# Optimization experiments

Hardware: AMD Instinct MI355X
Metric: run time of the kernel (lower is better)

Reference implementation:

```python
import jax, jax.numpy as jnp
import numpy as np

TEMPERATURE = 8.0  # sqrt(head_dim=64)


def sparsemax(z):
    """Sparsemax along the last axis (Martins & Astudillo 2016)."""
    S = z.shape[-1]
    z_sorted = -jnp.sort(-z, axis=-1)            # descending sort
    cs = jnp.cumsum(z_sorted, axis=-1)
    ks = jnp.arange(1, S + 1, dtype=z.dtype)
    support = 1.0 + ks * z_sorted > cs           # entries in the support set
    k_sup = jnp.sum(support, axis=-1, keepdims=True)  # support size >= 1
    tau = (jnp.take_along_axis(cs, k_sup - 1, axis=-1) - 1.0) / k_sup.astype(z.dtype)
    return jnp.maximum(z - tau, 0.0)


def setup_inputs() -> dict:
    key = jax.random.key(0)
    kq, kk, kv, km = jax.random.split(key, 4)
    B, Lq, Lk, D = 64, 1024, 1024, 64
    q = jax.random.normal(kq, (B, Lq, D), dtype=jnp.float32)
    k = jax.random.normal(kk, (B, Lk, D), dtype=jnp.float32)
    v = jax.random.normal(kv, (B, Lk, D), dtype=jnp.float32)
    mask = jax.random.randint(km, (B, Lq, Lk), 0, 2).astype(bool)  # True = masked out
    return {"q": q, "k": k, "v": v, "mask": mask}


def reference(q, k, v, mask):
    # scores: [B, Lq, Lk]
    attn = jnp.einsum('bqd,bkd->bqk', q / TEMPERATURE, k)
    # mask out disallowed keys with -inf
    attn = jnp.where(mask, -jnp.inf, attn)
    # rows where ALL keys are masked: set scores to 0 (avoids NaN in sparsemax)
    inf_mask = jnp.all(mask, axis=2, keepdims=True)  # [B, Lq, 1]
    attn = jnp.where(inf_mask, 0.0, attn)
    attn = sparsemax(attn)
    # zero out fully-masked rows again (dropout has p=0.0 -> identity in eval)
    attn = jnp.where(inf_mask, 0.0, attn)
    out = jnp.einsum('bqk,bkd->bqd', attn, v)
    return (out, attn)
```

## Files before the change

### kernel.cpp

```cpp
#include <hip/hip_runtime.h>
#include <float.h>


#define BATCH    64
#define SEQQ     1024
#define SEQK     1024
#define DHEAD    64

typedef short short8 __attribute__((ext_vector_type(8)));
typedef float f32x4  __attribute__((ext_vector_type(4)));
typedef unsigned short us4v __attribute__((ext_vector_type(4)));

typedef const __attribute__((address_space(1))) unsigned int as1_cuint;
typedef __attribute__((address_space(3))) unsigned int as3_uint;
typedef __attribute__((address_space(3))) unsigned char as3_uchar;

__device__ __forceinline__ unsigned short bf16_rne(float f) {
    unsigned u = __float_as_uint(f);
    u += 0x7fffu + ((u >> 16) & 1u);
    return (unsigned short)(u >> 16);
}

__device__ __forceinline__ void cvt_hilo8(const float* fv, float scale,
                                          short8* hi, short8* lo) {
    #pragma unroll
    for (int j = 0; j < 8; ++j) {
        float f = fv[j] * scale;
        unsigned short hb = bf16_rne(f);
        float hf = __uint_as_float((unsigned)hb << 16);
        (*hi)[j] = (short)hb;
        (*lo)[j] = (short)bf16_rne(f - hf);
    }
}

__global__ void detect_mask_fmt(const unsigned char* __restrict__ m,
                                int* __restrict__ flag) {
    __shared__ int s_found;
    if (threadIdx.x == 0) s_found = 0;
    __syncthreads();
    int found = 0;
    for (int o = threadIdx.x; o < 65536; o += 256) {
        if ((o & 3) != 0 && m[o] != 0) found = 1;
    }
    if (found) atomicOr(&s_found, 1);
    __syncthreads();
    if (threadIdx.x == 0) *flag = s_found;
}

__global__ __launch_bounds__(256) void kprep(
        const float* __restrict__ k, unsigned short* __restrict__ kbuf) {
    int gid  = blockIdx.x * 256 + threadIdx.x;
    int db   = gid & 7;
    int keyg = (gid >> 3) & 1023;
    int b    = gid >> 13;
    int kt   = keyg >> 7;
    int key  = keyg & 127;

    const float4* src =
        (const float4*)(k + ((size_t)b * SEQK + keyg) * DHEAD + db * 8);
    float4 f0 = src[0], f1 = src[1];
    float fv[8] = {f0.x, f0.y, f0.z, f0.w, f1.x, f1.y, f1.z, f1.w};
    short8 hi, lo;
    cvt_hilo8(fv, 1.0f, &hi, &lo);

    unsigned short* tile = kbuf + (size_t)(b * 8 + kt) * 16384;
    int off = key * 64 + ((db ^ (key & 7)) * 8);
    *(short8*)(tile + off)        = hi;
    *(short8*)(tile + 8192 + off) = lo;
}

__global__ __launch_bounds__(256) void score_kernel_dma(
        const float* __restrict__ q, const unsigned short* __restrict__ kbuf,
        unsigned short* __restrict__ sbuf, int pitch) {
    const int lane = threadIdx.x & 63;
    const int wave = threadIdx.x >> 6;
    const int quad = lane >> 4;
    const int l15  = lane & 15;
    const int qt = blockIdx.x >> 6;
    const int b  = blockIdx.x & 63;

    __shared__ unsigned short klds[2 * 128 * 64];

    const float* qrow =
        q + ((size_t)b * SEQQ + qt * 64 + wave * 16 + l15) * DHEAD;
    short8 a_hi[2], a_lo[2];
    #pragma unroll
    for (int kc = 0; kc < 2; ++kc) {
        const float4* src = (const float4*)(qrow + kc * 32 + quad * 8);
        float4 f0 = src[0], f1 = src[1];
        float fv[8] = {f0.x, f0.y, f0.z, f0.w, f1.x, f1.y, f1.z, f1.w};
        cvt_hilo8(fv, 0.125f, &a_hi[kc], &a_lo[kc]);
    }

    unsigned short* srow0 =
        sbuf + ((size_t)b * SEQQ + qt * 64 + wave * 16) * (size_t)pitch;

    for (int kt = 0; kt < 8; ++kt) {
        __syncthreads();
        const unsigned char* gtile =
            (const unsigned char*)(kbuf + (size_t)(b * 8 + kt) * 16384);
        {
            unsigned base = wave * 8192 + lane * 16;
            #pragma unroll
            for (int j = 0; j < 8; ++j) {
                unsigned off = base + j * 1024;
                as1_cuint* gp = (as1_cuint*)(gtile + off);
                as3_uint*  lp = (as3_uint*)((as3_uchar*)klds +
                                            (wave * 8192 + j * 1024));
                __builtin_amdgcn_global_load_lds(gp, lp, 16, 0, 0);
            }
        }
        __syncthreads();

        unsigned short* srow = srow0 + kt * 128;
        #pragma unroll
        for (int g = 0; g < 8; ++g) {
            int key = g * 16 + l15;
            short8 b_hi[2], b_lo[2];
            #pragma unroll
            for (int kc = 0; kc < 2; ++kc) {
                int db  = kc * 4 + quad;
                int off = key * 64 + ((db ^ (key & 7)) * 8);
                b_hi[kc] = *(const short8*)(klds + off);
                b_lo[kc] = *(const short8*)(klds + 8192 + off);
            }
            f32x4 acc = {0.f, 0.f, 0.f, 0.f};
            #pragma unroll
            for (int kc = 0; kc < 2; ++kc) {
                acc = __builtin_amdgcn_mfma_f32_16x16x32_bf16(a_hi[kc], b_hi[kc], acc, 0, 0, 0);
                acc = __builtin_amdgcn_mfma_f32_16x16x32_bf16(a_lo[kc], b_hi[kc], acc, 0, 0, 0);
                acc = __builtin_amdgcn_mfma_f32_16x16x32_bf16(a_hi[kc], b_lo[kc], acc, 0, 0, 0);
            }
            #pragma unroll
            for (int r = 0; r < 4; ++r)
                srow[(size_t)(quad * 4 + r) * (size_t)pitch + g * 16 + l15] =
                    bf16_rne(acc[r]);
        }
    }
}

__global__ __launch_bounds__(256) void score_kernel_cvt(
        const float* __restrict__ q, const float* __restrict__ k,
        unsigned short* __restrict__ sbuf, int pitch) {
    const int lane = threadIdx.x & 63;
    const int wave = threadIdx.x >> 6;
    const int quad = lane >> 4;
    const int l15  = lane & 15;
    const int qt = blockIdx.x >> 6;
    const int b  = blockIdx.x & 63;

    __shared__ unsigned short klds[2 * 128 * 64];

    const float* qrow =
        q + ((size_t)b * SEQQ + qt * 64 + wave * 16 + l15) * DHEAD;
    short8 a_hi[2], a_lo[2];
    #pragma unroll
    for (int kc = 0; kc < 2; ++kc) {
        const float4* src = (const float4*)(qrow + kc * 32 + quad * 8);
        float4 f0 = src[0], f1 = src[1];
        float fv[8] = {f0.x, f0.y, f0.z, f0.w, f1.x, f1.y, f1.z, f1.w};
        cvt_hilo8(fv, 0.125f, &a_hi[kc], &a_lo[kc]);
    }

    const float* kb = k + (size_t)b * SEQK * DHEAD;
    unsigned short* srow0 =
        sbuf + ((size_t)b * SEQQ + qt * 64 + wave * 16) * (size_t)pitch;

    for (int kt = 0; kt < 8; ++kt) {
        __syncthreads();
        const float* kbase = kb + (size_t)kt * 128 * DHEAD;
        #pragma unroll
        for (int it = 0; it < 4; ++it) {
            int e   = threadIdx.x + 256 * it;
            int key = e >> 3, db = e & 7;
            const float4* src = (const float4*)(kbase + key * DHEAD + db * 8);
            float4 f0 = src[0], f1 = src[1];
            float fv[8] = {f0.x, f0.y, f0.z, f0.w, f1.x, f1.y, f1.z, f1.w};
            short8 hi, lo;
            cvt_hilo8(fv, 1.0f, &hi, &lo);
            int off = key * 64 + ((db ^ (key & 7)) * 8);
            *(short8*)(klds + off)        = hi;
            *(short8*)(klds + 8192 + off) = lo;
        }
        __syncthreads();

        unsigned short* srow = srow0 + kt * 128;
        #pragma unroll
        for (int g = 0; g < 8; ++g) {
            int key = g * 16 + l15;
            short8 b_hi[2], b_lo[2];
            #pragma unroll
            for (int kc = 0; kc < 2; ++kc) {
                int db  = kc * 4 + quad;
                int off = key * 64 + ((db ^ (key & 7)) * 8);
                b_hi[kc] = *(const short8*)(klds + off);
                b_lo[kc] = *(const short8*)(klds + 8192 + off);
            }
            f32x4 acc = {0.f, 0.f, 0.f, 0.f};
            #pragma unroll
            for (int kc = 0; kc < 2; ++kc) {
                acc = __builtin_amdgcn_mfma_f32_16x16x32_bf16(a_hi[kc], b_hi[kc], acc, 0, 0, 0);
                acc = __builtin_amdgcn_mfma_f32_16x16x32_bf16(a_lo[kc], b_hi[kc], acc, 0, 0, 0);
                acc = __builtin_amdgcn_mfma_f32_16x16x32_bf16(a_hi[kc], b_lo[kc], acc, 0, 0, 0);
            }
            #pragma unroll
            for (int r = 0; r < 4; ++r)
                srow[(size_t)(quad * 4 + r) * (size_t)pitch + g * 16 + l15] =
                    bf16_rne(acc[r]);
        }
    }
}

__global__ __launch_bounds__(256) void sparsemax_pv(
        const float* __restrict__ v, const void* __restrict__ mask,
        const int* __restrict__ fmt_flag,
        float* __restrict__ out, float* __restrict__ attn,
        const unsigned short* __restrict__ sbuf, int pitch) {
    const int lane = threadIdx.x & 63;
    const int wave = threadIdx.x >> 6;
    const int row  = blockIdx.x * 4 + wave;
    const int b    = row >> 10;
    float* arow = attn + (size_t)row * SEQK;
    const int mask_is_byte = fmt_flag ? *fmt_flag : 1;

    __shared__ float pbuf[4][SEQK];

    const us4v* s4 = (const us4v*)(sbuf + (size_t)row * (size_t)pitch);
    float s[16];
    #pragma unroll
    for (int t = 0; t < 4; ++t) {
        us4v u = __builtin_nontemporal_load(s4 + lane + 64 * t);
        s[4*t+0] = __uint_as_float((unsigned)u[0] << 16);
        s[4*t+1] = __uint_as_float((unsigned)u[1] << 16);
        s[4*t+2] = __uint_as_float((unsigned)u[2] << 16);
        s[4*t+3] = __uint_as_float((unsigned)u[3] << 16);
    }
    if (mask_is_byte) {
        const unsigned* m32 =
            (const unsigned*)((const unsigned char*)mask + (size_t)row * SEQK);
        #pragma unroll
        for (int t = 0; t < 4; ++t) {
            unsigned m = __builtin_nontemporal_load(m32 + lane + 64 * t);
            if (m & 0x000000ffu) s[4*t+0] = -FLT_MAX;
            if (m & 0x0000ff00u) s[4*t+1] = -FLT_MAX;
            if (m & 0x00ff0000u) s[4*t+2] = -FLT_MAX;
            if (m & 0xff000000u) s[4*t+3] = -FLT_MAX;
        }
    } else {
        const int* mi = (const int*)mask + (size_t)row * SEQK;
        #pragma unroll
        for (int t = 0; t < 4; ++t) {
            int m0 = __builtin_nontemporal_load(mi + 4 * (lane + 64 * t) + 0);
            int m1 = __builtin_nontemporal_load(mi + 4 * (lane + 64 * t) + 1);
            int m2 = __builtin_nontemporal_load(mi + 4 * (lane + 64 * t) + 2);
            int m3 = __builtin_nontemporal_load(mi + 4 * (lane + 64 * t) + 3);
            if (m0) s[4*t+0] = -FLT_MAX;
            if (m1) s[4*t+1] = -FLT_MAX;
            if (m2) s[4*t+2] = -FLT_MAX;
            if (m3) s[4*t+3] = -FLT_MAX;
        }
    }

    float mx = -FLT_MAX;
    #pragma unroll
    for (int i = 0; i < 16; ++i) mx = fmaxf(mx, s[i]);
    #pragma unroll
    for (int off = 32; off >= 1; off >>= 1)
        mx = fmaxf(mx, __shfl_xor(mx, off, 64));

    if (mx <= -FLT_MAX) {
        f32x4 z = {0.f, 0.f, 0.f, 0.f};
        #pragma unroll
        for (int t = 0; t < 4; ++t)
            __builtin_nontemporal_store(z, (f32x4*)arow + lane + 64 * t);
        out[(size_t)row * DHEAD + lane] = 0.f;
        return;
    }

    float thr = mx - 1.0f, tau = 0.f;
    int cnt_prev = -1;
    for (int it = 0; it < 32; ++it) {
        float lsum = 0.f; int lcnt = 0;
        #pragma unroll
        for (int i = 0; i < 16; ++i)
            if (s[i] > thr) { lsum += s[i]; lcnt++; }
        #pragma unroll
        for (int off = 32; off >= 1; off >>= 1) {
            lsum += __shfl_xor(lsum, off, 64);
            lcnt += __shfl_xor(lcnt, off, 64);
        }
        tau = (lsum - 1.0f) / (float)lcnt;
        if (lcnt == cnt_prev) break;
        cnt_prev = lcnt;
        thr = tau;
    }

    float p[16];
    #pragma unroll
    for (int i = 0; i < 16; ++i) {
        float pv = s[i] - tau;
        p[i] = pv > 0.f ? pv : 0.f;
    }
    #pragma unroll
    for (int t = 0; t < 4; ++t) {
        f32x4 f = {p[4*t+0], p[4*t+1], p[4*t+2], p[4*t+3]};
        __builtin_nontemporal_store(f, (f32x4*)arow + lane + 64 * t);
        *(f32x4*)&pbuf[wave][4 * (lane + 64 * t)] = f;
    }

    const float* vbase = v + (size_t)b * SEQK * DHEAD;
    float oacc = 0.f;
    #pragma unroll
    for (int t = 0; t < 4; ++t) {
        #pragma unroll
        for (int c = 0; c < 4; ++c) {
            int i = 4 * t + c;
            unsigned long long mb = __ballot(p[i] > 0.f);
            while (mb) {
                int k0, k1 = -1, k2 = -1, k3 = -1;
                k0 = __ffsll(mb) - 1; mb &= mb - 1;
                if (mb) { k1 = __ffsll(mb) - 1; mb &= mb - 1; }
                if (mb) { k2 = __ffsll(mb) - 1; mb &= mb - 1; }
                if (mb) { k3 = __ffsll(mb) - 1; mb &= mb - 1; }
                int key0 = 4 * k0 + 256 * t + c;
                float pj0 = pbuf[wave][key0];
                float v0  = vbase[(size_t)key0 * DHEAD + lane];
                float pj1 = 0.f, pj2 = 0.f, pj3 = 0.f;
                float v1 = 0.f, v2 = 0.f, v3 = 0.f;
                if (k1 >= 0) {
                    int key1 = 4 * k1 + 256 * t + c;
                    pj1 = pbuf[wave][key1];
                    v1  = vbase[(size_t)key1 * DHEAD + lane];
                }
                if (k2 >= 0) {
                    int key2 = 4 * k2 + 256 * t + c;
                    pj2 = pbuf[wave][key2];
                    v2  = vbase[(size_t)key2 * DHEAD + lane];
                }
                if (k3 >= 0) {
                    int key3 = 4 * k3 + 256 * t + c;
                    pj3 = pbuf[wave][key3];
                    v3  = vbase[(size_t)key3 * DHEAD + lane];
                }
                oacc = fmaf(pj0, v0, oacc);
                if (k1 >= 0) oacc = fmaf(pj1, v1, oacc);
                if (k2 >= 0) oacc = fmaf(pj2, v2, oacc);
                if (k3 >= 0) oacc = fmaf(pj3, v3, oacc);
            }
        }
    }
    out[(size_t)row * DHEAD + lane] = oacc;
}

extern "C" void kernel_launch(void* const* d_in, const int* in_sizes, int n_in,
                              void* d_out, int out_size, void* d_ws, size_t ws_size,
                              hipStream_t stream) {
    const float* q = (const float*)d_in[0];
    const float* k = (const float*)d_in[1];
    const float* v = (const float*)d_in[2];
    const void*  m = d_in[3];

    float* out  = (float*)d_out;
    float* attn = out + (size_t)BATCH * SEQQ * DHEAD;

    int* flag = nullptr;
    if (ws_size >= sizeof(int)) {
        flag = (int*)d_ws;
        detect_mask_fmt<<<1, 256, 0, stream>>>((const unsigned char*)m, flag);
    }

    const size_t S_BYTES = (size_t)BATCH * SEQQ * SEQK * 2;
    const size_t K_BYTES = (size_t)BATCH * SEQK * DHEAD * 2 * 2;

    unsigned short* sbuf;
    int pitch;
    bool s_in_ws = ws_size >= 16 + S_BYTES;
    if (s_in_ws) {
        sbuf  = (unsigned short*)d_ws + 8;
        pitch = SEQK;
    } else {
        sbuf  = (unsigned short*)attn;
        pitch = 2 * SEQK;
    }

    bool k_in_ws = s_in_ws && ws_size >= 16 + S_BYTES + K_BYTES;
    if (k_in_ws) {
        unsigned short* kbuf =
            (unsigned short*)((char*)d_ws + 16 + S_BYTES);
        kprep<<<(BATCH * SEQK * 8) / 256, 256, 0, stream>>>(k, kbuf);
        score_kernel_dma<<<(SEQQ / 64) * BATCH, 256, 0, stream>>>(
            q, kbuf, sbuf, pitch);
    } else {
        score_kernel_cvt<<<(SEQQ / 64) * BATCH, 256, 0, stream>>>(
            q, k, sbuf, pitch);
    }

    sparsemax_pv<<<(BATCH * SEQQ) / 4, 256, 0, stream>>>(
        v, m, flag, out, attn, sbuf, pitch);
}
```

Before: 646.2 us.

## Transpose score MFMA for packed stores and write sparse attn over memset

The score kernels swap the MFMA operand order so each lane holds four consecutive keys for one query row, which allows a packed 8-byte bf16 store instead of four strided 2-byte stores. When the score buffer lives in the workspace, the attention output is cleared with a hipMemsetAsync and the sparsemax kernel writes only the nonzero probabilities with scattered scalar stores, instead of dense nontemporal vector stores of the full row. This replaces kernel-side zero writes with a driver fill pass. The scattered per-element stores may coalesce poorly.

```diff
diff --git a/kernel.cpp b/kernel.cpp
--- a/kernel.cpp
+++ b/kernel.cpp
@@ -83,17 +83,17 @@
 
     const float* qrow =
         q + ((size_t)b * SEQQ + qt * 64 + wave * 16 + l15) * DHEAD;
-    short8 a_hi[2], a_lo[2];
+    short8 q_hi[2], q_lo[2];
     #pragma unroll
     for (int kc = 0; kc < 2; ++kc) {
         const float4* src = (const float4*)(qrow + kc * 32 + quad * 8);
         float4 f0 = src[0], f1 = src[1];
         float fv[8] = {f0.x, f0.y, f0.z, f0.w, f1.x, f1.y, f1.z, f1.w};
-        cvt_hilo8(fv, 0.125f, &a_hi[kc], &a_lo[kc]);
-    }
-
-    unsigned short* srow0 =
-        sbuf + ((size_t)b * SEQQ + qt * 64 + wave * 16) * (size_t)pitch;
+        cvt_hilo8(fv, 0.125f, &q_hi[kc], &q_lo[kc]);
+    }
+
+    unsigned short* srow =
+        sbuf + ((size_t)b * SEQQ + qt * 64 + wave * 16 + l15) * (size_t)pitch;
 
     for (int kt = 0; kt < 8; ++kt) {
         __syncthreads();
@@ -112,29 +112,27 @@
         }
         __syncthreads();
 
-        unsigned short* srow = srow0 + kt * 128;
         #pragma unroll
         for (int g = 0; g < 8; ++g) {
             int key = g * 16 + l15;
-            short8 b_hi[2], b_lo[2];
+            short8 k_hi[2], k_lo[2];
             #pragma unroll
             for (int kc = 0; kc < 2; ++kc) {
                 int db  = kc * 4 + quad;
                 int off = key * 64 + ((db ^ (key & 7)) * 8);
-                b_hi[kc] = *(const short8*)(klds + off);
-                b_lo[kc] = *(const short8*)(klds + 8192 + off);
+                k_hi[kc] = *(const short8*)(klds + off);
+                k_lo[kc] = *(const short8*)(klds + 8192 + off);
             }
             f32x4 acc = {0.f, 0.f, 0.f, 0.f};
             #pragma unroll
             for (int kc = 0; kc < 2; ++kc) {
-                acc = __builtin_amdgcn_mfma_f32_16x16x32_bf16(a_hi[kc], b_hi[kc], acc, 0, 0, 0);
-                acc = __builtin_amdgcn_mfma_f32_16x16x32_bf16(a_lo[kc], b_hi[kc], acc, 0, 0, 0);
-                acc = __builtin_amdgcn_mfma_f32_16x16x32_bf16(a_hi[kc], b_lo[kc], acc, 0, 0, 0);
-            }
-            #pragma unroll
-            for (int r = 0; r < 4; ++r)
-                srow[(size_t)(quad * 4 + r) * (size_t)pitch + g * 16 + l15] =
-                    bf16_rne(acc[r]);
+                acc = __builtin_amdgcn_mfma_f32_16x16x32_bf16(k_hi[kc], q_hi[kc], acc, 0, 0, 0);
+                acc = __builtin_amdgcn_mfma_f32_16x16x32_bf16(k_hi[kc], q_lo[kc], acc, 0, 0, 0);
+                acc = __builtin_amdgcn_mfma_f32_16x16x32_bf16(k_lo[kc], q_hi[kc], acc, 0, 0, 0);
+            }
+            us4v pk = {bf16_rne(acc[0]), bf16_rne(acc[1]),
+                       bf16_rne(acc[2]), bf16_rne(acc[3])};
+            *(us4v*)(srow + kt * 128 + g * 16 + quad * 4) = pk;
         }
     }
 }
@@ -153,18 +151,18 @@
 
     const float* qrow =
         q + ((size_t)b * SEQQ + qt * 64 + wave * 16 + l15) * DHEAD;
-    short8 a_hi[2], a_lo[2];
+    short8 q_hi[2], q_lo[2];
     #pragma unroll
     for (int kc = 0; kc < 2; ++kc) {
         const float4* src = (const float4*)(qrow + kc * 32 + quad * 8);
         float4 f0 = src[0], f1 = src[1];
         float fv[8] = {f0.x, f0.y, f0.z, f0.w, f1.x, f1.y, f1.z, f1.w};
-        cvt_hilo8(fv, 0.125f, &a_hi[kc], &a_lo[kc]);
+        cvt_hilo8(fv, 0.125f, &q_hi[kc], &q_lo[kc]);
     }
 
     const float* kb = k + (size_t)b * SEQK * DHEAD;
-    unsigned short* srow0 =
-        sbuf + ((size_t)b * SEQQ + qt * 64 + wave * 16) * (size_t)pitch;
+    unsigned short* srow =
+        sbuf + ((size_t)b * SEQQ + qt * 64 + wave * 16 + l15) * (size_t)pitch;
 
     for (int kt = 0; kt < 8; ++kt) {
         __syncthreads();
@@ -184,29 +182,27 @@
         }
         __syncthreads();
 
-        unsigned short* srow = srow0 + kt * 128;
         #pragma unroll
         for (int g = 0; g < 8; ++g) {
             int key = g * 16 + l15;
-            short8 b_hi[2], b_lo[2];
+            short8 k_hi[2], k_lo[2];
             #pragma unroll
             for (int kc = 0; kc < 2; ++kc) {
                 int db  = kc * 4 + quad;
                 int off = key * 64 + ((db ^ (key & 7)) * 8);
-                b_hi[kc] = *(const short8*)(klds + off);
-                b_lo[kc] = *(const short8*)(klds + 8192 + off);
+                k_hi[kc] = *(const short8*)(klds + off);
+                k_lo[kc] = *(const short8*)(klds + 8192 + off);
             }
             f32x4 acc = {0.f, 0.f, 0.f, 0.f};
             #pragma unroll
             for (int kc = 0; kc < 2; ++kc) {
-                acc = __builtin_amdgcn_mfma_f32_16x16x32_bf16(a_hi[kc], b_hi[kc], acc, 0, 0, 0);
-                acc = __builtin_amdgcn_mfma_f32_16x16x32_bf16(a_lo[kc], b_hi[kc], acc, 0, 0, 0);
-                acc = __builtin_amdgcn_mfma_f32_16x16x32_bf16(a_hi[kc], b_lo[kc], acc, 0, 0, 0);
-            }
-            #pragma unroll
-            for (int r = 0; r < 4; ++r)
-                srow[(size_t)(quad * 4 + r) * (size_t)pitch + g * 16 + l15] =
-                    bf16_rne(acc[r]);
+                acc = __builtin_amdgcn_mfma_f32_16x16x32_bf16(k_hi[kc], q_hi[kc], acc, 0, 0, 0);
+                acc = __builtin_amdgcn_mfma_f32_16x16x32_bf16(k_hi[kc], q_lo[kc], acc, 0, 0, 0);
+                acc = __builtin_amdgcn_mfma_f32_16x16x32_bf16(k_lo[kc], q_hi[kc], acc, 0, 0, 0);
+            }
+            us4v pk = {bf16_rne(acc[0]), bf16_rne(acc[1]),
+                       bf16_rne(acc[2]), bf16_rne(acc[3])};
+            *(us4v*)(srow + kt * 128 + g * 16 + quad * 4) = pk;
         }
     }
 }
@@ -215,7 +211,7 @@
         const float* __restrict__ v, const void* __restrict__ mask,
         const int* __restrict__ fmt_flag,
         float* __restrict__ out, float* __restrict__ attn,
-        const unsigned short* __restrict__ sbuf, int pitch) {
+        const unsigned short* __restrict__ sbuf, int pitch, int full_write) {
     const int lane = threadIdx.x & 63;
     const int wave = threadIdx.x >> 6;
     const int row  = blockIdx.x * 4 + wave;
@@ -269,10 +265,12 @@
         mx = fmaxf(mx, __shfl_xor(mx, off, 64));
 
     if (mx <= -FLT_MAX) {
-        f32x4 z = {0.f, 0.f, 0.f, 0.f};
-        #pragma unroll
-        for (int t = 0; t < 4; ++t)
-            __builtin_nontemporal_store(z, (f32x4*)arow + lane + 64 * t);
+        if (full_write) {
+            f32x4 z = {0.f, 0.f, 0.f, 0.f};
+            #pragma unroll
+            for (int t = 0; t < 4; ++t)
+                __builtin_nontemporal_store(z, (f32x4*)arow + lane + 64 * t);
+        }
         out[(size_t)row * DHEAD + lane] = 0.f;
         return;
     }
@@ -304,8 +302,19 @@
     #pragma unroll
     for (int t = 0; t < 4; ++t) {
         f32x4 f = {p[4*t+0], p[4*t+1], p[4*t+2], p[4*t+3]};
-        __builtin_nontemporal_store(f, (f32x4*)arow + lane + 64 * t);
+        if (full_write)
+            __builtin_nontemporal_store(f, (f32x4*)arow + lane + 64 * t);
         *(f32x4*)&pbuf[wave][4 * (lane + 64 * t)] = f;
+    }
+    if (!full_write) {
+        #pragma unroll
+        for (int t = 0; t < 4; ++t) {
+            #pragma unroll
+            for (int c = 0; c < 4; ++c) {
+                float pv = p[4*t+c];
+                if (pv > 0.f) arow[4 * (lane + 64 * t) + c] = pv;
+            }
+        }
     }
 
     const float* vbase = v + (size_t)b * SEQK * DHEAD;
@@ -378,6 +387,8 @@
     if (s_in_ws) {
         sbuf  = (unsigned short*)d_ws + 8;
         pitch = SEQK;
+        hipMemsetAsync(attn, 0, (size_t)BATCH * SEQQ * SEQK * sizeof(float),
+                       stream);
     } else {
         sbuf  = (unsigned short*)attn;
         pitch = 2 * SEQK;
@@ -396,5 +407,5 @@
     }
 
     sparsemax_pv<<<(BATCH * SEQQ) / 4, 256, 0, stream>>>(
-        v, m, flag, out, attn, sbuf, pitch);
-}
+        v, m, flag, out, attn, sbuf, pitch, s_in_ws ? 0 : 1);
+}
```

Measured after the change: 667.4 us. +3.3%, slower.
